# Optimization experiments

Hardware: AMD Instinct MI355X
Metric: run time of the kernel (lower is better)

Reference implementation:

```python
import jax, jax.numpy as jnp
import numpy as np

N_NODES = 100000
N_EDGES = 1600000
IN_FEATS = 128
HIDDEN = 128
N_CLASSES = 47


def setup_inputs() -> dict:
    key = jax.random.key(0)
    ks = jax.random.split(key, 8)
    x = jax.random.normal(ks[0], (N_NODES, IN_FEATS), dtype=jnp.float32)
    edges = jax.random.randint(ks[1], (2, N_EDGES), 0, N_NODES, dtype=jnp.int32)
    W0 = jax.random.normal(ks[2], (IN_FEATS, HIDDEN), dtype=jnp.float32) * (1.0 / np.sqrt(IN_FEATS))
    b0 = jnp.zeros((HIDDEN,), dtype=jnp.float32)
    W1 = jax.random.normal(ks[3], (HIDDEN, HIDDEN), dtype=jnp.float32) * (1.0 / np.sqrt(HIDDEN))
    b1 = jnp.zeros((HIDDEN,), dtype=jnp.float32)
    Wc = jax.random.normal(ks[4], (HIDDEN, N_CLASSES), dtype=jnp.float32) * (1.0 / np.sqrt(HIDDEN))
    bc = jnp.zeros((N_CLASSES,), dtype=jnp.float32)
    return {"x": x, "edges": edges, "W0": W0, "b0": b0, "W1": W1, "b1": b1, "Wc": Wc, "bc": bc}


def reference(x, edges, W0, b0, W1, b1, Wc, bc):
    N = x.shape[0]
    src, dst = edges[0], edges[1]
    ones = jnp.ones((src.shape[0],), dtype=x.dtype)
    # symmetric 'both' normalization: out-degree for src, in-degree for dst (clamped to >=1)
    out_deg = jax.ops.segment_sum(ones, src, num_segments=N)
    in_deg = jax.ops.segment_sum(ones, dst, num_segments=N)
    c_src = jnp.maximum(out_deg, 1.0) ** -0.5  # [N]
    c_dst = jnp.maximum(in_deg, 1.0) ** -0.5   # [N]

    def graph_conv(h, W, b):
        h = (h * c_src[:, None]) @ W                       # dense transform [N, H]
        h = jax.ops.segment_sum(h[src], dst, num_segments=N)  # sparse SpMM aggregation
        h = h * c_dst[:, None] + b
        return jax.nn.relu(h)

    h = graph_conv(x, W0, b0)
    h = graph_conv(h, W1, b1)
    return h @ Wc + bc
```

## Files before the change

### kernel.cpp

```cpp
#include <hip/hip_runtime.h>
#include <hip/hip_fp16.h>


#define PB 256
#define BSHIFT 8

typedef _Float16 f16x8 __attribute__((ext_vector_type(8)));
typedef float f32x4 __attribute__((ext_vector_type(4)));


__global__ __launch_bounds__(256) void k_count(const int* __restrict__ src, const int* __restrict__ dst,
                                               int E, int per_blk, int NB,
                                               int* __restrict__ cntT, int* __restrict__ cntT2) {
  __shared__ int cnt[512];
  __shared__ int cnt2[512];
  for (int i = threadIdx.x; i < NB; i += 256) { cnt[i] = 0; cnt2[i] = 0; }
  __syncthreads();
  int e0 = blockIdx.x * per_blk, e1 = min(E, e0 + per_blk);
  for (int e = e0 + threadIdx.x; e < e1; e += 256) {
    atomicAdd(&cnt[dst[e] >> BSHIFT], 1);
    atomicAdd(&cnt2[src[e] >> BSHIFT], 1);
  }
  __syncthreads();
  for (int i = threadIdx.x; i < NB; i += 256) {
    cntT[i * PB + blockIdx.x] = cnt[i];
    cntT2[i * PB + blockIdx.x] = cnt2[i];
  }
}

__global__ __launch_bounds__(256) void k_scanblk(const int* __restrict__ cntT, int* __restrict__ offsT,
                                                 int* __restrict__ total) {
  __shared__ int s[256];
  int b = blockIdx.x, t = threadIdx.x;
  int v = cntT[b * PB + t];
  s[t] = v;
  __syncthreads();
  for (int off = 1; off < 256; off <<= 1) {
    int x = (t >= off) ? s[t - off] : 0;
    __syncthreads();
    s[t] += x;
    __syncthreads();
  }
  offsT[b * PB + t] = s[t] - v;
  if (t == 255) total[b] = s[255];
}

__global__ __launch_bounds__(512) void k_scantot(const int* __restrict__ total, int NB, int E,
                                                 int* __restrict__ bbase, int* __restrict__ sbase,
                                                 int* __restrict__ row_ptr, int N) {
  __shared__ int s[512];
  int t = threadIdx.x;
  const int* tot = (blockIdx.x == 0) ? total : total + NB;
  int* obase = (blockIdx.x == 0) ? bbase : sbase;
  int v = (t < NB) ? tot[t] : 0;
  s[t] = v;
  __syncthreads();
  for (int off = 1; off < 512; off <<= 1) {
    int x = (t >= off) ? s[t - off] : 0;
    __syncthreads();
    s[t] += x;
    __syncthreads();
  }
  if (t < NB) obase[t] = s[t] - v;
  if (t == 0) obase[NB] = E;
  if (blockIdx.x == 0 && t == 0) row_ptr[N] = E;
}


__global__ __launch_bounds__(256) void k_partition(const int* __restrict__ src, const int* __restrict__ dst,
                                                   int E, int per_blk, int NB,
                                                   const int* __restrict__ offsT, const int* __restrict__ bbase,
                                                   const int* __restrict__ offsT2, const int* __restrict__ sbase,
                                                   unsigned* __restrict__ ebuf, unsigned char* __restrict__ sbuf,
                                                   int src_bits) {
  __shared__ int cur[512];
  __shared__ int cur2[512];
  for (int i = threadIdx.x; i < NB; i += 256) {
    cur[i] = bbase[i] + offsT[i * PB + blockIdx.x];
    cur2[i] = sbase[i] + offsT2[i * PB + blockIdx.x];
  }
  __syncthreads();
  int e0 = blockIdx.x * per_blk, e1 = min(E, e0 + per_blk);
  for (int e = e0 + threadIdx.x; e < e1; e += 256) {
    int d = dst[e], s = src[e];
    int pos = atomicAdd(&cur[d >> BSHIFT], 1);
    ebuf[pos] = ((unsigned)(d & ((1 << BSHIFT) - 1)) << src_bits) | (unsigned)s;
    int pos2 = atomicAdd(&cur2[s >> BSHIFT], 1);
    sbuf[pos2] = (unsigned char)(s & ((1 << BSHIFT) - 1));
  }
}


__global__ __launch_bounds__(256) void k_finalize(const unsigned* __restrict__ ebuf, const int* __restrict__ bbase,
                                                  int N, int src_bits, int* __restrict__ row_ptr,
                                                  float* __restrict__ c_dst, int* __restrict__ col_idx,
                                                  const unsigned char* __restrict__ sbuf,
                                                  const int* __restrict__ sbase, float* __restrict__ c_src) {
  __shared__ int cnt[256];
  __shared__ int s[256];
  __shared__ int cur[256];
  int b = blockIdx.x, t = threadIdx.x;
  int r0 = bbase[b], r1 = bbase[b + 1];
  cnt[t] = 0;
  __syncthreads();
  for (int i = r0 + t; i < r1; i += 256) atomicAdd(&cnt[ebuf[i] >> src_bits], 1);
  __syncthreads();
  int v = cnt[t];
  s[t] = v;
  __syncthreads();
  for (int off = 1; off < 256; off <<= 1) {
    int x = (t >= off) ? s[t - off] : 0;
    __syncthreads();
    s[t] += x;
    __syncthreads();
  }
  int ex = s[t] - v;
  cur[t] = ex;
  int node = (b << BSHIFT) + t;
  if (node < N) {
    row_ptr[node] = r0 + ex;
    c_dst[node] = rsqrtf((float)max(v, 1));
  }
  __syncthreads();
  unsigned smask = (1u << src_bits) - 1u;
  for (int i = r0 + t; i < r1; i += 256) {
    unsigned e = ebuf[i];
    int pos = r0 + atomicAdd(&cur[e >> src_bits], 1);
    col_idx[pos] = (int)((e & smask) << 8);
  }
  __syncthreads();
  cnt[t] = 0;
  __syncthreads();
  int q0 = sbase[b], q1 = sbase[b + 1];
  for (int i = q0 + t; i < q1; i += 256) atomicAdd(&cnt[sbuf[i]], 1);
  __syncthreads();
  if (node < N) c_src[node] = rsqrtf((float)max(cnt[t], 1));
}


__device__ __forceinline__ f16x8 load_af(const float* arow, int off, float csc) {
  float4 a0 = *(const float4*)(arow + off);
  float4 a1 = *(const float4*)(arow + off + 4);
  f16x8 v;
  v[0] = (_Float16)(a0.x * csc);
  v[1] = (_Float16)(a0.y * csc);
  v[2] = (_Float16)(a0.z * csc);
  v[3] = (_Float16)(a0.w * csc);
  v[4] = (_Float16)(a1.x * csc);
  v[5] = (_Float16)(a1.y * csc);
  v[6] = (_Float16)(a1.z * csc);
  v[7] = (_Float16)(a1.w * csc);
  return v;
}

__device__ __forceinline__ f16x8 load_af(const __half* arow, int off, float csc) {
  f16x8 v = *(const f16x8*)(arow + off);
  _Float16 c = (_Float16)csc;
#pragma unroll
  for (int j = 0; j < 8; j++) v[j] = v[j] * c;
  return v;
}

template <typename AT>
__global__ __launch_bounds__(256) void k_gemm_mfma(const AT* __restrict__ A, const float* __restrict__ W,
                                                   const float* __restrict__ scale, __half* __restrict__ out, int N) {
  __shared__ _Float16 Wt[128][136];
  int t = threadIdx.x;
  {
    int nlow = t & 15;
    int kplow = t >> 4;
#pragma unroll
    for (int j = 0; j < 32; j++) {
      int n = nlow + 16 * (j & 7);
      int kp = kplow + 16 * (j >> 3);
      float w0 = W[(size_t)(2 * kp) * 128 + n];
      float w1 = W[(size_t)(2 * kp + 1) * 128 + n];
      __half2 h2 = __floats2half2_rn(w0, w1);
      *(__half2*)&Wt[n][2 * kp] = h2;
    }
  }
  __syncthreads();

  int wave = t >> 6;
  int lane = t & 63;
  int li = lane & 15;
  int q = lane >> 4;

#pragma unroll
  for (int s2 = 0; s2 < 2; s2++) {
    int m0 = (blockIdx.x * 2 + s2) * 128 + wave * 32;
    if (m0 >= N) break;

    int mrow[2];
    float csc[2];
    bool mok[2];
    const AT* arow[2];
#pragma unroll
    for (int s = 0; s < 2; s++) {
      mrow[s] = m0 + s * 16 + li;
      mok[s] = mrow[s] < N;
      csc[s] = mok[s] ? scale[mrow[s]] : 0.f;
      arow[s] = A + (size_t)(mok[s] ? mrow[s] : 0) * 128;
    }

    f32x4 acc[2][8];
#pragma unroll
    for (int s = 0; s < 2; s++)
#pragma unroll
      for (int nt = 0; nt < 8; nt++) acc[s][nt] = (f32x4){0.f, 0.f, 0.f, 0.f};

#pragma unroll
    for (int kc = 0; kc < 128; kc += 32) {
      f16x8 af[2];
#pragma unroll
      for (int s = 0; s < 2; s++) af[s] = load_af(arow[s], kc + q * 8, csc[s]);
#pragma unroll
      for (int nt = 0; nt < 8; nt++) {
        f16x8 wf = *(const f16x8*)&Wt[nt * 16 + li][kc + q * 8];
        acc[0][nt] = __builtin_amdgcn_mfma_f32_16x16x32_f16(wf, af[0], acc[0][nt], 0, 0, 0);
        acc[1][nt] = __builtin_amdgcn_mfma_f32_16x16x32_f16(wf, af[1], acc[1][nt], 0, 0, 0);
      }
    }

#pragma unroll
    for (int s = 0; s < 2; s++) {
      if (!mok[s]) continue;
      size_t rb = (size_t)mrow[s] * 128;
#pragma unroll
      for (int nt = 0; nt < 8; nt++) {
        __half2 p0 = __floats2half2_rn(acc[s][nt][0], acc[s][nt][1]);
        __half2 p1 = __floats2half2_rn(acc[s][nt][2], acc[s][nt][3]);
        uint2 qv;
        qv.x = *(unsigned*)&p0;
        qv.y = *(unsigned*)&p1;
        *(uint2*)&out[rb + nt * 16 + q * 4] = qv;
      }
    }
  }
}


__device__ __forceinline__ void acc_pair(float4& a, uint2 qa, uint2 qb) {
  __half2 s0 = __hadd2(*(__half2*)&qa.x, *(__half2*)&qb.x);
  __half2 s1 = __hadd2(*(__half2*)&qa.y, *(__half2*)&qb.y);
  float2 f0 = __half22float2(s0);
  float2 f1 = __half22float2(s1);
  a.x += f0.x; a.y += f0.y; a.z += f1.x; a.w += f1.y;
}

__device__ __forceinline__ void acc_one(float4& a, uint2 q) {
  float2 f0 = __half22float2(*(__half2*)&q.x);
  float2 f1 = __half22float2(*(__half2*)&q.y);
  a.x += f0.x; a.y += f0.y; a.z += f1.x; a.w += f1.y;
}

__global__ __launch_bounds__(256) void k_aggregate_h(const __half* __restrict__ hin, const int* __restrict__ rp,
                                                     const int* __restrict__ ci, const float* __restrict__ c_dst,
                                                     const float* __restrict__ bias, __half* __restrict__ hout, int N) {
  int v = blockIdx.x * 4 + (threadIdx.x >> 6);
  if (v >= N) return;
  int half_id = (threadIdx.x >> 5) & 1;
  int f4 = (threadIdx.x & 31) * 4;
  const char* hb = (const char*)hin + f4 * 2;
  int p0 = rp[v], pe = rp[v + 1];
  int mid = p0 + ((pe - p0 + 1) >> 1);
  int p = half_id ? mid : p0;
  int pend = half_id ? pe : mid;
  float4 a0 = make_float4(0.f, 0.f, 0.f, 0.f);
  float4 a1 = make_float4(0.f, 0.f, 0.f, 0.f);
  float4 a2 = make_float4(0.f, 0.f, 0.f, 0.f);
  float4 a3 = make_float4(0.f, 0.f, 0.f, 0.f);
  for (; p + 7 < pend; p += 8) {
    int u0 = ci[p];
    int u1 = ci[p + 1];
    int u2 = ci[p + 2];
    int u3 = ci[p + 3];
    int u4 = ci[p + 4];
    int u5 = ci[p + 5];
    int u6 = ci[p + 6];
    int u7 = ci[p + 7];
    uint2 q0 = *(const uint2*)(hb + (size_t)(unsigned)u0);
    uint2 q1 = *(const uint2*)(hb + (size_t)(unsigned)u1);
    uint2 q2 = *(const uint2*)(hb + (size_t)(unsigned)u2);
    uint2 q3 = *(const uint2*)(hb + (size_t)(unsigned)u3);
    uint2 q4 = *(const uint2*)(hb + (size_t)(unsigned)u4);
    uint2 q5 = *(const uint2*)(hb + (size_t)(unsigned)u5);
    uint2 q6 = *(const uint2*)(hb + (size_t)(unsigned)u6);
    uint2 q7 = *(const uint2*)(hb + (size_t)(unsigned)u7);
    acc_pair(a0, q0, q1);
    acc_pair(a1, q2, q3);
    acc_pair(a2, q4, q5);
    acc_pair(a3, q6, q7);
  }
  for (; p + 1 < pend; p += 2) {
    int u0 = ci[p];
    int u1 = ci[p + 1];
    uint2 q0 = *(const uint2*)(hb + (size_t)(unsigned)u0);
    uint2 q1 = *(const uint2*)(hb + (size_t)(unsigned)u1);
    acc_pair(a0, q0, q1);
  }
  if (p < pend) {
    uint2 q = *(const uint2*)(hb + (size_t)(unsigned)ci[p]);
    acc_one(a0, q);
  }
  a0.x += a1.x; a0.y += a1.y; a0.z += a1.z; a0.w += a1.w;
  a2.x += a3.x; a2.y += a3.y; a2.z += a3.z; a2.w += a3.w;
  a0.x += a2.x; a0.y += a2.y; a0.z += a2.z; a0.w += a2.w;
  a0.x += __shfl_xor(a0.x, 32);
  a0.y += __shfl_xor(a0.y, 32);
  a0.z += __shfl_xor(a0.z, 32);
  a0.w += __shfl_xor(a0.w, 32);
  if (half_id == 0) {
    float cd = c_dst[v];
    float4 b = *(const float4*)&bias[f4];
    float4 o;
    o.x = fmaxf(fmaf(a0.x, cd, b.x), 0.f);
    o.y = fmaxf(fmaf(a0.y, cd, b.y), 0.f);
    o.z = fmaxf(fmaf(a0.z, cd, b.z), 0.f);
    o.w = fmaxf(fmaf(a0.w, cd, b.w), 0.f);
    __half2 p0h = __floats2half2_rn(o.x, o.y);
    __half2 p1h = __floats2half2_rn(o.z, o.w);
    uint2 qv;
    qv.x = *(unsigned*)&p0h;
    qv.y = *(unsigned*)&p1h;
    *(uint2*)&hout[(size_t)v * 128 + f4] = qv;
  }
}


__global__ __launch_bounds__(256) void k_classifier_mfma(const __half* __restrict__ h, const float* __restrict__ Wc,
                                                         const float* __restrict__ bc, float* __restrict__ out, int N) {
  __shared__ _Float16 Wt[96][136];
  __shared__ float bs[48];
  int t = threadIdx.x;
  if (t < 47) bs[t] = bc[t];
  if (t == 47) bs[47] = 0.f;
  for (int i = t; i < 48 * 128; i += 256) {
    int n = i >> 7, k = i & 127;
    float w = (n < 47) ? Wc[(size_t)k * 47 + n] : 0.f;
    _Float16 hi = (_Float16)w;
    Wt[n][k] = hi;
    Wt[n + 48][k] = (_Float16)(w - (float)hi);
  }
  __syncthreads();

  int wave = t >> 6;
  int lane = t & 63;
  int li = lane & 15;
  int q = lane >> 4;

#pragma unroll
  for (int s2 = 0; s2 < 2; s2++) {
    int m0 = (blockIdx.x * 2 + s2) * 128 + wave * 32;
    if (m0 >= N) break;

    int mrow[2];
    bool mok[2];
    const __half* arow[2];
#pragma unroll
    for (int s = 0; s < 2; s++) {
      mrow[s] = m0 + s * 16 + li;
      mok[s] = mrow[s] < N;
      arow[s] = h + (size_t)(mok[s] ? mrow[s] : 0) * 128;
    }

    f32x4 acc[2][3];
#pragma unroll
    for (int s = 0; s < 2; s++)
#pragma unroll
      for (int nt = 0; nt < 3; nt++) acc[s][nt] = (f32x4){0.f, 0.f, 0.f, 0.f};

#pragma unroll
    for (int kc = 0; kc < 128; kc += 32) {
      f16x8 af[2];
#pragma unroll
      for (int s = 0; s < 2; s++) af[s] = *(const f16x8*)(arow[s] + kc + q * 8);
#pragma unroll
      for (int nt = 0; nt < 3; nt++) {
        f16x8 whi = *(const f16x8*)&Wt[nt * 16 + li][kc + q * 8];
        f16x8 wlo = *(const f16x8*)&Wt[48 + nt * 16 + li][kc + q * 8];
        acc[0][nt] = __builtin_amdgcn_mfma_f32_16x16x32_f16(whi, af[0], acc[0][nt], 0, 0, 0);
        acc[1][nt] = __builtin_amdgcn_mfma_f32_16x16x32_f16(whi, af[1], acc[1][nt], 0, 0, 0);
        acc[0][nt] = __builtin_amdgcn_mfma_f32_16x16x32_f16(wlo, af[0], acc[0][nt], 0, 0, 0);
        acc[1][nt] = __builtin_amdgcn_mfma_f32_16x16x32_f16(wlo, af[1], acc[1][nt], 0, 0, 0);
      }
    }

#pragma unroll
    for (int s = 0; s < 2; s++) {
      if (!mok[s]) continue;
      size_t rb = (size_t)mrow[s] * 47;
#pragma unroll
      for (int nt = 0; nt < 3; nt++) {
#pragma unroll
        for (int j = 0; j < 4; j++) {
          int c = nt * 16 + q * 4 + j;
          if (c < 47) out[rb + c] = acc[s][nt][j] + bs[c];
        }
      }
    }
  }
}


extern "C" void kernel_launch(void* const* d_in, const int* in_sizes, int n_in,
                              void* d_out, int out_size, void* d_ws, size_t ws_size,
                              hipStream_t stream) {
  const float* x  = (const float*)d_in[0];
  const int* edges = (const int*)d_in[1];
  const float* W0 = (const float*)d_in[2];
  const float* b0 = (const float*)d_in[3];
  const float* W1 = (const float*)d_in[4];
  const float* b1 = (const float*)d_in[5];
  const float* Wc = (const float*)d_in[6];
  const float* bc = (const float*)d_in[7];
  float* out = (float*)d_out;

  int N = in_sizes[0] / 128;
  int E = in_sizes[1] / 2;
  const int* src = edges;
  const int* dst = edges + E;

  int NB = (N + ((1 << BSHIFT) - 1)) >> BSHIFT;
  int src_bits = 0;
  while ((1 << src_bits) < N) src_bits++;
  int per_blk = (E + PB - 1) / PB;

  char* base = (char*)d_ws;
  size_t off = 0;
  auto alloc = [&](size_t bytes) -> void* {
    void* p = base + off;
    off += (bytes + 255) & ~(size_t)255;
    return p;
  };
  float* c_src = (float*)alloc((size_t)N * 4);
  float* c_dst = (float*)alloc((size_t)N * 4);
  int* row_ptr = (int*)alloc((size_t)(N + 1) * 4);
  int* col_idx = (int*)alloc((size_t)E * 4);
  __half* h0h = (__half*)alloc((size_t)N * 128 * 2);
  __half* h1h = (__half*)alloc((size_t)N * 128 * 2);

  char* hb = (char*)h1h;
  unsigned* ebuf = (unsigned*)hb;            hb += (size_t)E * 4;
  unsigned char* sbuf = (unsigned char*)hb;  hb += ((size_t)E + 255) & ~(size_t)255;
  int* cntT = (int*)hb;                      hb += (size_t)2 * NB * PB * 4;
  int* offsT = (int*)hb;                     hb += (size_t)2 * NB * PB * 4;
  int* total = (int*)hb;                     hb += (size_t)2 * NB * 4;
  int* bbase = (int*)hb;                     hb += (size_t)(NB + 1) * 4;
  int* sbase = (int*)hb;                     hb += (size_t)(NB + 1) * 4;
  int* cntT2 = cntT + (size_t)NB * PB;
  int* offsT2 = offsT + (size_t)NB * PB;

  k_count<<<PB, 256, 0, stream>>>(src, dst, E, per_blk, NB, cntT, cntT2);
  k_scanblk<<<2 * NB, 256, 0, stream>>>(cntT, offsT, total);
  k_scantot<<<2, 512, 0, stream>>>(total, NB, E, bbase, sbase, row_ptr, N);
  k_partition<<<PB, 256, 0, stream>>>(src, dst, E, per_blk, NB, offsT, bbase, offsT2, sbase,
                                      ebuf, sbuf, src_bits);
  k_finalize<<<NB, 256, 0, stream>>>(ebuf, bbase, N, src_bits, row_ptr, c_dst, col_idx,
                                     sbuf, sbase, c_src);

  int strips = (N + 127) / 128;
  int gblocks = (strips + 1) / 2;
  k_gemm_mfma<float><<<gblocks, 256, 0, stream>>>(x, W0, c_src, h0h, N);
  k_aggregate_h<<<(N + 3) / 4, 256, 0, stream>>>(h0h, row_ptr, col_idx, c_dst, b0, h1h, N);
  k_gemm_mfma<__half><<<gblocks, 256, 0, stream>>>(h1h, W1, c_src, h0h, N);
  k_aggregate_h<<<(N + 3) / 4, 256, 0, stream>>>(h0h, row_ptr, col_idx, c_dst, b1, h1h, N);
  k_classifier_mfma<<<gblocks, 256, 0, stream>>>(h1h, Wc, bc, out, N);
}
```

Measured before the change: 345.8 us.

## Build CSR with global-atomic degree counts and per-node fill instead of bucket partition

Replaces the two-level bucketed counting sort (per-block bucket histograms, partition into buffers, per-bucket finalize) with a direct CSR build. Degrees come from global atomics, are scanned per node, and each edge is placed by a global atomic cursor per destination. This removes several passes and the intermediate buffers. The cost is heavier contention on global atomics, and the order of neighbours within each row is no longer deterministic.

```diff
diff --git a/kernel.cpp b/kernel.cpp
--- a/kernel.cpp
+++ b/kernel.cpp
@@ -2,38 +2,32 @@
 #include <hip/hip_fp16.h>
 
 
-#define PB 256
+#define EB 1024
 #define BSHIFT 8
 
 typedef _Float16 f16x8 __attribute__((ext_vector_type(8)));
 typedef float f32x4 __attribute__((ext_vector_type(4)));
 
 
-__global__ __launch_bounds__(256) void k_count(const int* __restrict__ src, const int* __restrict__ dst,
-                                               int E, int per_blk, int NB,
-                                               int* __restrict__ cntT, int* __restrict__ cntT2) {
-  __shared__ int cnt[512];
-  __shared__ int cnt2[512];
-  for (int i = threadIdx.x; i < NB; i += 256) { cnt[i] = 0; cnt2[i] = 0; }
-  __syncthreads();
-  int e0 = blockIdx.x * per_blk, e1 = min(E, e0 + per_blk);
-  for (int e = e0 + threadIdx.x; e < e1; e += 256) {
-    atomicAdd(&cnt[dst[e] >> BSHIFT], 1);
-    atomicAdd(&cnt2[src[e] >> BSHIFT], 1);
-  }
-  __syncthreads();
-  for (int i = threadIdx.x; i < NB; i += 256) {
-    cntT[i * PB + blockIdx.x] = cnt[i];
-    cntT2[i * PB + blockIdx.x] = cnt2[i];
-  }
-}
-
-__global__ __launch_bounds__(256) void k_scanblk(const int* __restrict__ cntT, int* __restrict__ offsT,
-                                                 int* __restrict__ total) {
+__global__ __launch_bounds__(256) void k_degcnt(const int* __restrict__ edges, int twoE, int E, int per_blk,
+                                                int* __restrict__ deg_out, int* __restrict__ deg_in) {
+  int i0 = blockIdx.x * per_blk, i1 = min(twoE, i0 + per_blk);
+  for (int i = i0 + threadIdx.x; i < i1; i += 256) {
+    int v = edges[i];
+    int* d = (i < E) ? deg_out : deg_in;
+    atomicAdd(&d[v], 1);
+  }
+}
+
+
+__global__ __launch_bounds__(256) void k_scanvals(const int* __restrict__ deg_in, const int* __restrict__ deg_out,
+                                                  int N, float* __restrict__ c_dst, float* __restrict__ c_src,
+                                                  int* __restrict__ lex, int* __restrict__ bsum) {
   __shared__ int s[256];
   int b = blockIdx.x, t = threadIdx.x;
-  int v = cntT[b * PB + t];
-  s[t] = v;
+  int node = (b << BSHIFT) + t;
+  int d = (node < N) ? deg_in[node] : 0;
+  s[t] = d;
   __syncthreads();
   for (int off = 1; off < 256; off <<= 1) {
     int x = (t >= off) ? s[t - off] : 0;
@@ -41,18 +35,20 @@
     s[t] += x;
     __syncthreads();
   }
-  offsT[b * PB + t] = s[t] - v;
-  if (t == 255) total[b] = s[255];
-}
-
-__global__ __launch_bounds__(512) void k_scantot(const int* __restrict__ total, int NB, int E,
-                                                 int* __restrict__ bbase, int* __restrict__ sbase,
-                                                 int* __restrict__ row_ptr, int N) {
+  lex[node] = s[t] - d;
+  if (t == 255) bsum[b] = s[255];
+  if (node < N) {
+    c_dst[node] = rsqrtf((float)max(d, 1));
+    c_src[node] = rsqrtf((float)max(deg_out[node], 1));
+  }
+}
+
+
+__global__ __launch_bounds__(512) void k_scantot(const int* __restrict__ bsum, int NB, int E,
+                                                 int* __restrict__ bbase, int* __restrict__ row_ptr, int N) {
   __shared__ int s[512];
   int t = threadIdx.x;
-  const int* tot = (blockIdx.x == 0) ? total : total + NB;
-  int* obase = (blockIdx.x == 0) ? bbase : sbase;
-  int v = (t < NB) ? tot[t] : 0;
+  int v = (t < NB) ? bsum[t] : 0;
   s[t] = v;
   __syncthreads();
   for (int off = 1; off < 512; off <<= 1) {
@@ -61,80 +57,34 @@
     s[t] += x;
     __syncthreads();
   }
-  if (t < NB) obase[t] = s[t] - v;
-  if (t == 0) obase[NB] = E;
-  if (blockIdx.x == 0 && t == 0) row_ptr[N] = E;
-}
-
-
-__global__ __launch_bounds__(256) void k_partition(const int* __restrict__ src, const int* __restrict__ dst,
-                                                   int E, int per_blk, int NB,
-                                                   const int* __restrict__ offsT, const int* __restrict__ bbase,
-                                                   const int* __restrict__ offsT2, const int* __restrict__ sbase,
-                                                   unsigned* __restrict__ ebuf, unsigned char* __restrict__ sbuf,
-                                                   int src_bits) {
-  __shared__ int cur[512];
-  __shared__ int cur2[512];
-  for (int i = threadIdx.x; i < NB; i += 256) {
-    cur[i] = bbase[i] + offsT[i * PB + blockIdx.x];
-    cur2[i] = sbase[i] + offsT2[i * PB + blockIdx.x];
-  }
-  __syncthreads();
+  if (t < NB) bbase[t] = s[t] - v;
+  if (t == 0) {
+    bbase[NB] = E;
+    row_ptr[N] = E;
+  }
+}
+
+
+__global__ __launch_bounds__(256) void k_scatter_rp(const int* __restrict__ bbase, const int* __restrict__ lex,
+                                                    int N, int* __restrict__ row_ptr, int* __restrict__ cur) {
+  int node = (blockIdx.x << BSHIFT) + threadIdx.x;
+  if (node < N) {
+    int rp = bbase[blockIdx.x] + lex[node];
+    row_ptr[node] = rp;
+    cur[node] = rp;
+  }
+}
+
+
+__global__ __launch_bounds__(256) void k_fill(const int* __restrict__ src, const int* __restrict__ dst,
+                                              int E, int per_blk, int* __restrict__ cur,
+                                              int* __restrict__ col_idx) {
   int e0 = blockIdx.x * per_blk, e1 = min(E, e0 + per_blk);
   for (int e = e0 + threadIdx.x; e < e1; e += 256) {
     int d = dst[e], s = src[e];
-    int pos = atomicAdd(&cur[d >> BSHIFT], 1);
-    ebuf[pos] = ((unsigned)(d & ((1 << BSHIFT) - 1)) << src_bits) | (unsigned)s;
-    int pos2 = atomicAdd(&cur2[s >> BSHIFT], 1);
-    sbuf[pos2] = (unsigned char)(s & ((1 << BSHIFT) - 1));
-  }
-}
-
-
-__global__ __launch_bounds__(256) void k_finalize(const unsigned* __restrict__ ebuf, const int* __restrict__ bbase,
-                                                  int N, int src_bits, int* __restrict__ row_ptr,
-                                                  float* __restrict__ c_dst, int* __restrict__ col_idx,
-                                                  const unsigned char* __restrict__ sbuf,
-                                                  const int* __restrict__ sbase, float* __restrict__ c_src) {
-  __shared__ int cnt[256];
-  __shared__ int s[256];
-  __shared__ int cur[256];
-  int b = blockIdx.x, t = threadIdx.x;
-  int r0 = bbase[b], r1 = bbase[b + 1];
-  cnt[t] = 0;
-  __syncthreads();
-  for (int i = r0 + t; i < r1; i += 256) atomicAdd(&cnt[ebuf[i] >> src_bits], 1);
-  __syncthreads();
-  int v = cnt[t];
-  s[t] = v;
-  __syncthreads();
-  for (int off = 1; off < 256; off <<= 1) {
-    int x = (t >= off) ? s[t - off] : 0;
-    __syncthreads();
-    s[t] += x;
-    __syncthreads();
-  }
-  int ex = s[t] - v;
-  cur[t] = ex;
-  int node = (b << BSHIFT) + t;
-  if (node < N) {
-    row_ptr[node] = r0 + ex;
-    c_dst[node] = rsqrtf((float)max(v, 1));
-  }
-  __syncthreads();
-  unsigned smask = (1u << src_bits) - 1u;
-  for (int i = r0 + t; i < r1; i += 256) {
-    unsigned e = ebuf[i];
-    int pos = r0 + atomicAdd(&cur[e >> src_bits], 1);
-    col_idx[pos] = (int)((e & smask) << 8);
-  }
-  __syncthreads();
-  cnt[t] = 0;
-  __syncthreads();
-  int q0 = sbase[b], q1 = sbase[b + 1];
-  for (int i = q0 + t; i < q1; i += 256) atomicAdd(&cnt[sbuf[i]], 1);
-  __syncthreads();
-  if (node < N) c_src[node] = rsqrtf((float)max(cnt[t], 1));
+    int pos = atomicAdd(&cur[d], 1);
+    col_idx[pos] = s << 8;
+  }
 }
 
 
@@ -422,9 +372,8 @@
   const int* dst = edges + E;
 
   int NB = (N + ((1 << BSHIFT) - 1)) >> BSHIFT;
-  int src_bits = 0;
-  while ((1 << src_bits) < N) src_bits++;
-  int per_blk = (E + PB - 1) / PB;
+  int per_blk2 = (2 * E + EB - 1) / EB;
+  int per_blk = (E + EB - 1) / EB;
 
   char* base = (char*)d_ws;
   size_t off = 0;
@@ -441,23 +390,20 @@
   __half* h1h = (__half*)alloc((size_t)N * 128 * 2);
 
   char* hb = (char*)h1h;
-  unsigned* ebuf = (unsigned*)hb;            hb += (size_t)E * 4;
-  unsigned char* sbuf = (unsigned char*)hb;  hb += ((size_t)E + 255) & ~(size_t)255;
-  int* cntT = (int*)hb;                      hb += (size_t)2 * NB * PB * 4;
-  int* offsT = (int*)hb;                     hb += (size_t)2 * NB * PB * 4;
-  int* total = (int*)hb;                     hb += (size_t)2 * NB * 4;
+  int* deg = (int*)hb;                       hb += (size_t)2 * N * 4;
+  int* lex = (int*)hb;                       hb += (size_t)NB * 256 * 4;
+  int* bsum = (int*)hb;                      hb += (size_t)NB * 4;
   int* bbase = (int*)hb;                     hb += (size_t)(NB + 1) * 4;
-  int* sbase = (int*)hb;                     hb += (size_t)(NB + 1) * 4;
-  int* cntT2 = cntT + (size_t)NB * PB;
-  int* offsT2 = offsT + (size_t)NB * PB;
-
-  k_count<<<PB, 256, 0, stream>>>(src, dst, E, per_blk, NB, cntT, cntT2);
-  k_scanblk<<<2 * NB, 256, 0, stream>>>(cntT, offsT, total);
-  k_scantot<<<2, 512, 0, stream>>>(total, NB, E, bbase, sbase, row_ptr, N);
-  k_partition<<<PB, 256, 0, stream>>>(src, dst, E, per_blk, NB, offsT, bbase, offsT2, sbase,
-                                      ebuf, sbuf, src_bits);
-  k_finalize<<<NB, 256, 0, stream>>>(ebuf, bbase, N, src_bits, row_ptr, c_dst, col_idx,
-                                     sbuf, sbase, c_src);
+  int* cur = (int*)hb;                       hb += (size_t)N * 4;
+  int* deg_out = deg;
+  int* deg_in = deg + N;
+
+  hipMemsetAsync(deg, 0, (size_t)2 * N * 4, stream);
+  k_degcnt<<<EB, 256, 0, stream>>>(edges, 2 * E, E, per_blk2, deg_out, deg_in);
+  k_scanvals<<<NB, 256, 0, stream>>>(deg_in, deg_out, N, c_dst, c_src, lex, bsum);
+  k_scantot<<<1, 512, 0, stream>>>(bsum, NB, E, bbase, row_ptr, N);
+  k_scatter_rp<<<NB, 256, 0, stream>>>(bbase, lex, N, row_ptr, cur);
+  k_fill<<<EB, 256, 0, stream>>>(src, dst, E, per_blk, cur, col_idx);
 
   int strips = (N + 127) / 128;
   int gblocks = (strips + 1) / 2;
```

After: 543.9 us. +57.3%, slower.

## Fuse CSR finalize with first GEMM in one heterogeneous launch

Applied to the files above, without the earlier changes.

Splits the finalize kernel into a small out-degree pass that produces c_src and a dst-CSR build. The CSR build now runs as extra blocks inside the first MFMA GEMM launch, reusing the GEMM's shared memory. This lets the CSR construction overlap with the first dense transform, which only needs c_src, and removes one kernel boundary. The cost is an extra small launch for c_src and a more complex kernel with mixed block roles.

```diff
diff --git a/kernel.cpp b/kernel.cpp
--- a/kernel.cpp
+++ b/kernel.cpp
@@ -14,7 +14,7 @@
                                                int* __restrict__ cntT, int* __restrict__ cntT2) {
   __shared__ int cnt[512];
   __shared__ int cnt2[512];
-  for (int i = threadIdx.x; i < NB; i += 256) { cnt[i] = 0; cnt2[i] = 0; }
+  for (int i = threadIdx.x; i < 512; i += 256) { cnt[i] = 0; cnt2[i] = 0; }
   __syncthreads();
   int e0 = blockIdx.x * per_blk, e1 = min(E, e0 + per_blk);
   for (int e = e0 + threadIdx.x; e < e1; e += 256) {
@@ -91,81 +91,67 @@
 }
 
 
-__global__ __launch_bounds__(256) void k_finalize(const unsigned* __restrict__ ebuf, const int* __restrict__ bbase,
-                                                  int N, int src_bits, int* __restrict__ row_ptr,
-                                                  float* __restrict__ c_dst, int* __restrict__ col_idx,
-                                                  const unsigned char* __restrict__ sbuf,
-                                                  const int* __restrict__ sbase, float* __restrict__ c_src) {
+__global__ __launch_bounds__(256) void k_finalize_src(const unsigned char* __restrict__ sbuf,
+                                                      const int* __restrict__ sbase, int N,
+                                                      float* __restrict__ c_src) {
   __shared__ int cnt[256];
-  __shared__ int s[256];
-  __shared__ int cur[256];
   int b = blockIdx.x, t = threadIdx.x;
-  int r0 = bbase[b], r1 = bbase[b + 1];
-  cnt[t] = 0;
-  __syncthreads();
-  for (int i = r0 + t; i < r1; i += 256) atomicAdd(&cnt[ebuf[i] >> src_bits], 1);
-  __syncthreads();
-  int v = cnt[t];
-  s[t] = v;
-  __syncthreads();
-  for (int off = 1; off < 256; off <<= 1) {
-    int x = (t >= off) ? s[t - off] : 0;
-    __syncthreads();
-    s[t] += x;
-    __syncthreads();
-  }
-  int ex = s[t] - v;
-  cur[t] = ex;
-  int node = (b << BSHIFT) + t;
-  if (node < N) {
-    row_ptr[node] = r0 + ex;
-    c_dst[node] = rsqrtf((float)max(v, 1));
-  }
-  __syncthreads();
-  unsigned smask = (1u << src_bits) - 1u;
-  for (int i = r0 + t; i < r1; i += 256) {
-    unsigned e = ebuf[i];
-    int pos = r0 + atomicAdd(&cur[e >> src_bits], 1);
-    col_idx[pos] = (int)((e & smask) << 8);
-  }
-  __syncthreads();
   cnt[t] = 0;
   __syncthreads();
   int q0 = sbase[b], q1 = sbase[b + 1];
   for (int i = q0 + t; i < q1; i += 256) atomicAdd(&cnt[sbuf[i]], 1);
   __syncthreads();
+  int node = (b << BSHIFT) + t;
   if (node < N) c_src[node] = rsqrtf((float)max(cnt[t], 1));
 }
 
 
-__device__ __forceinline__ f16x8 load_af(const float* arow, int off, float csc) {
-  float4 a0 = *(const float4*)(arow + off);
-  float4 a1 = *(const float4*)(arow + off + 4);
-  f16x8 v;
-  v[0] = (_Float16)(a0.x * csc);
-  v[1] = (_Float16)(a0.y * csc);
-  v[2] = (_Float16)(a0.z * csc);
-  v[3] = (_Float16)(a0.w * csc);
-  v[4] = (_Float16)(a1.x * csc);
-  v[5] = (_Float16)(a1.y * csc);
-  v[6] = (_Float16)(a1.z * csc);
-  v[7] = (_Float16)(a1.w * csc);
-  return v;
-}
-
-__device__ __forceinline__ f16x8 load_af(const __half* arow, int off, float csc) {
-  f16x8 v = *(const f16x8*)(arow + off);
-  _Float16 c = (_Float16)csc;
-#pragma unroll
-  for (int j = 0; j < 8; j++) v[j] = v[j] * c;
-  return v;
-}
-
-template <typename AT>
-__global__ __launch_bounds__(256) void k_gemm_mfma(const AT* __restrict__ A, const float* __restrict__ W,
-                                                   const float* __restrict__ scale, __half* __restrict__ out, int N) {
+__global__ __launch_bounds__(256) void k_fin_gemm(const unsigned* __restrict__ ebuf, const int* __restrict__ bbase,
+                                                  int N, int src_bits, int NB,
+                                                  int* __restrict__ row_ptr, float* __restrict__ c_dst,
+                                                  int* __restrict__ col_idx,
+                                                  const float* __restrict__ A, const float* __restrict__ W,
+                                                  const float* __restrict__ scale, __half* __restrict__ out) {
   __shared__ _Float16 Wt[128][136];
   int t = threadIdx.x;
+
+  if (blockIdx.x < NB) {
+    int* cnt = (int*)&Wt[0][0];
+    int* s = cnt + 256;
+    int* cur = cnt + 512;
+    int b = blockIdx.x;
+    int r0 = bbase[b], r1 = bbase[b + 1];
+    cnt[t] = 0;
+    __syncthreads();
+    for (int i = r0 + t; i < r1; i += 256) atomicAdd(&cnt[ebuf[i] >> src_bits], 1);
+    __syncthreads();
+    int v = cnt[t];
+    s[t] = v;
+    __syncthreads();
+    for (int off = 1; off < 256; off <<= 1) {
+      int x = (t >= off) ? s[t - off] : 0;
+      __syncthreads();
+      s[t] += x;
+      __syncthreads();
+    }
+    int ex = s[t] - v;
+    cur[t] = ex;
+    int node = (b << BSHIFT) + t;
+    if (node < N) {
+      row_ptr[node] = r0 + ex;
+      c_dst[node] = rsqrtf((float)max(v, 1));
+    }
+    __syncthreads();
+    unsigned smask = (1u << src_bits) - 1u;
+    for (int i = r0 + t; i < r1; i += 256) {
+      unsigned e = ebuf[i];
+      int pos = r0 + atomicAdd(&cur[e >> src_bits], 1);
+      col_idx[pos] = (int)((e & smask) << 8);
+    }
+    return;
+  }
+
+  int bid = blockIdx.x - NB;
   {
     int nlow = t & 15;
     int kplow = t >> 4;
@@ -188,13 +174,112 @@
 
 #pragma unroll
   for (int s2 = 0; s2 < 2; s2++) {
-    int m0 = (blockIdx.x * 2 + s2) * 128 + wave * 32;
+    int m0 = (bid * 2 + s2) * 128 + wave * 32;
     if (m0 >= N) break;
 
     int mrow[2];
     float csc[2];
     bool mok[2];
-    const AT* arow[2];
+    const float* arow[2];
+#pragma unroll
+    for (int s = 0; s < 2; s++) {
+      mrow[s] = m0 + s * 16 + li;
+      mok[s] = mrow[s] < N;
+      csc[s] = mok[s] ? scale[mrow[s]] : 0.f;
+      arow[s] = A + (size_t)(mok[s] ? mrow[s] : 0) * 128;
+    }
+
+    f32x4 acc[2][8];
+#pragma unroll
+    for (int s = 0; s < 2; s++)
+#pragma unroll
+      for (int nt = 0; nt < 8; nt++) acc[s][nt] = (f32x4){0.f, 0.f, 0.f, 0.f};
+
+#pragma unroll
+    for (int kc = 0; kc < 128; kc += 32) {
+      f16x8 af[2];
+#pragma unroll
+      for (int s = 0; s < 2; s++) {
+        float4 a0 = *(const float4*)(arow[s] + kc + q * 8);
+        float4 a1 = *(const float4*)(arow[s] + kc + q * 8 + 4);
+        f16x8 v;
+        v[0] = (_Float16)(a0.x * csc[s]);
+        v[1] = (_Float16)(a0.y * csc[s]);
+        v[2] = (_Float16)(a0.z * csc[s]);
+        v[3] = (_Float16)(a0.w * csc[s]);
+        v[4] = (_Float16)(a1.x * csc[s]);
+        v[5] = (_Float16)(a1.y * csc[s]);
+        v[6] = (_Float16)(a1.z * csc[s]);
+        v[7] = (_Float16)(a1.w * csc[s]);
+        af[s] = v;
+      }
+#pragma unroll
+      for (int nt = 0; nt < 8; nt++) {
+        f16x8 wf = *(const f16x8*)&Wt[nt * 16 + li][kc + q * 8];
+        acc[0][nt] = __builtin_amdgcn_mfma_f32_16x16x32_f16(wf, af[0], acc[0][nt], 0, 0, 0);
+        acc[1][nt] = __builtin_amdgcn_mfma_f32_16x16x32_f16(wf, af[1], acc[1][nt], 0, 0, 0);
+      }
+    }
+
+#pragma unroll
+    for (int s = 0; s < 2; s++) {
+      if (!mok[s]) continue;
+      size_t rb = (size_t)mrow[s] * 128;
+#pragma unroll
+      for (int nt = 0; nt < 8; nt++) {
+        __half2 p0 = __floats2half2_rn(acc[s][nt][0], acc[s][nt][1]);
+        __half2 p1 = __floats2half2_rn(acc[s][nt][2], acc[s][nt][3]);
+        uint2 qv;
+        qv.x = *(unsigned*)&p0;
+        qv.y = *(unsigned*)&p1;
+        *(uint2*)&out[rb + nt * 16 + q * 4] = qv;
+      }
+    }
+  }
+}
+
+
+__device__ __forceinline__ f16x8 load_af(const __half* arow, int off, float csc) {
+  f16x8 v = *(const f16x8*)(arow + off);
+  _Float16 c = (_Float16)csc;
+#pragma unroll
+  for (int j = 0; j < 8; j++) v[j] = v[j] * c;
+  return v;
+}
+
+__global__ __launch_bounds__(256) void k_gemm_mfma_h(const __half* __restrict__ A, const float* __restrict__ W,
+                                                     const float* __restrict__ scale, __half* __restrict__ out, int N) {
+  __shared__ _Float16 Wt[128][136];
+  int t = threadIdx.x;
+  {
+    int nlow = t & 15;
+    int kplow = t >> 4;
+#pragma unroll
+    for (int j = 0; j < 32; j++) {
+      int n = nlow + 16 * (j & 7);
+      int kp = kplow + 16 * (j >> 3);
+      float w0 = W[(size_t)(2 * kp) * 128 + n];
+      float w1 = W[(size_t)(2 * kp + 1) * 128 + n];
+      __half2 h2 = __floats2half2_rn(w0, w1);
+      *(__half2*)&Wt[n][2 * kp] = h2;
+    }
+  }
+  __syncthreads();
+
+  int wave = t >> 6;
+  int lane = t & 63;
+  int li = lane & 15;
+  int q = lane >> 4;
+
+#pragma unroll
+  for (int s2 = 0; s2 < 2; s2++) {
+    int m0 = (blockIdx.x * 2 + s2) * 128 + wave * 32;
+    if (m0 >= N) break;
+
+    int mrow[2];
+    float csc[2];
+    bool mok[2];
+    const __half* arow[2];
 #pragma unroll
     for (int s = 0; s < 2; s++) {
       mrow[s] = m0 + s * 16 + li;
@@ -456,14 +541,15 @@
   k_scantot<<<2, 512, 0, stream>>>(total, NB, E, bbase, sbase, row_ptr, N);
   k_partition<<<PB, 256, 0, stream>>>(src, dst, E, per_blk, NB, offsT, bbase, offsT2, sbase,
                                       ebuf, sbuf, src_bits);
-  k_finalize<<<NB, 256, 0, stream>>>(ebuf, bbase, N, src_bits, row_ptr, c_dst, col_idx,
-                                     sbuf, sbase, c_src);
+  k_finalize_src<<<NB, 256, 0, stream>>>(sbuf, sbase, N, c_src);
 
   int strips = (N + 127) / 128;
   int gblocks = (strips + 1) / 2;
-  k_gemm_mfma<float><<<gblocks, 256, 0, stream>>>(x, W0, c_src, h0h, N);
+  k_fin_gemm<<<NB + gblocks, 256, 0, stream>>>(ebuf, bbase, N, src_bits, NB,
+                                               row_ptr, c_dst, col_idx,
+                                               x, W0, c_src, h0h);
   k_aggregate_h<<<(N + 3) / 4, 256, 0, stream>>>(h0h, row_ptr, col_idx, c_dst, b0, h1h, N);
-  k_gemm_mfma<__half><<<gblocks, 256, 0, stream>>>(h1h, W1, c_src, h0h, N);
+  k_gemm_mfma_h<<<gblocks, 256, 0, stream>>>(h1h, W1, c_src, h0h, N);
   k_aggregate_h<<<(N + 3) / 4, 256, 0, stream>>>(h0h, row_ptr, col_idx, c_dst, b1, h1h, N);
   k_classifier_mfma<<<gblocks, 256, 0, stream>>>(h1h, Wc, bc, out, N);
 }
```

Result: no change. 344.6 us (-0.3%).
